# Kernel optimization log

Measured on AMD Instinct MI355X. Metric: run time of the kernel, lower is better.

The kernel has to match this reference:

```python
import jax, jax.numpy as jnp
import numpy as np

NEG_BIG = -9e15
ALPHA = 0.2  # LeakyReLU negative slope
B, N, F_IN, F_OUT = 8, 2048, 128, 128


def setup_inputs() -> dict:
    key = jax.random.key(0)
    k1, k2, k3, k4 = jax.random.split(key, 4)
    inp = jax.random.normal(k1, (B, N, F_IN), dtype=jnp.float32)
    adj = jax.random.randint(k2, (B, N, N), 0, 2, dtype=jnp.int32)
    W = 0.02 * jax.random.normal(k3, (F_OUT, F_IN), dtype=jnp.float32)  # nn.Linear weight [out,in]
    a = 0.02 * jax.random.normal(k4, (1, 2 * F_OUT), dtype=jnp.float32)  # attention vector [1, 2F]
    return {"input": inp, "adj": adj, "W": W, "a": a}


def reference(input, adj, W, a):
    # h = input @ W^T : [B, N, F_OUT]
    h = jnp.einsum("bnf,of->bno", input, W)
    f_out = h.shape[-1]
    # Decompose a . [h_i || h_j] = (h_i . a1) + (h_j . a2) -- same math as the
    # explicit repeat_interleave/repeat/cat, without the O(N^2 * 2F) tensor.
    a1 = a[0, :f_out]
    a2 = a[0, f_out:]
    s1 = h @ a1  # [B, N] score for source node i
    s2 = h @ a2  # [B, N] score for target node j
    e = jax.nn.leaky_relu(s1[:, :, None] + s2[:, None, :], negative_slope=ALPHA)  # [B,N,N]
    masked = jnp.where(adj > 0, e, NEG_BIG)
    attention = jax.nn.softmax(masked, axis=-1)
    # dropout p=0.0 (eval) -> identity
    h_prime = jnp.einsum("bnm,bmo->bno", attention, h)
    return h_prime
```

## Files before the change

### kernel.cpp

```cpp
#include <hip/hip_runtime.h>
#include <stdint.h>


#define B_ 8
#define N_ 2048
#define FD 128
#define ALPHA_ 0.2f
#define TJ 32
#define NCH 16
#define CHU4 512

typedef __attribute__((ext_vector_type(8))) short short8;
typedef __attribute__((ext_vector_type(4))) float f32x4;

#define HCHUNK(o, jc) ((((o) * 16) + ((jc) ^ ((o) & 15))) * 8)
#define U32(o, jc) (((o) >> 1) * 8 + ((((((o) & 1) << 2)) | (jc)) ^ (((o) >> 1) & 7)))

__device__ __forceinline__ float bf2f(unsigned short u) {
    union { uint32_t i; float f; } v; v.i = ((uint32_t)u) << 16; return v.f;
}
__device__ __forceinline__ unsigned short f2bf(float f) {
    union { float f; uint32_t i; } v; v.f = f;
    uint32_t x = v.i;
    uint32_t r = (x + 0x7fffu + ((x >> 16) & 1u)) >> 16;
    return (unsigned short)r;
}

__device__ __forceinline__ void gl2lds16(const uint4* g, uint4* l) {
    __builtin_amdgcn_global_load_lds(
        (const __attribute__((address_space(1))) uint32_t*)g,
        (__attribute__((address_space(3))) uint32_t*)l, 16, 0, 0);
}

__global__ __launch_bounds__(256) void gat_h(
    const float* __restrict__ x,
    const float* __restrict__ W,
    const float* __restrict__ a,
    unsigned short* __restrict__ hT,
    float* __restrict__ s1o, float* __restrict__ s2o)
{
    __shared__ __align__(16) unsigned short Wlds[FD * FD];

    const int bid = blockIdx.x;
    const int tid = threadIdx.x;
    const int w = tid >> 6;
    const int lane = tid & 63;
    const int m = lane & 15;
    const int quad = lane >> 4;
    const int arow = bid * 64 + w * 16 + m;

#pragma unroll
    for (int it = 0; it < 8; it++) {
        int cid = it * 256 + tid;
        int o = cid >> 4, kc = cid & 15;
        const float* wp = W + (size_t)o * FD + kc * 8;
        float4 w0 = *(const float4*)wp;
        float4 w1 = *(const float4*)(wp + 4);
        uint4 pk;
        pk.x = (uint32_t)f2bf(w0.x) | ((uint32_t)f2bf(w0.y) << 16);
        pk.y = (uint32_t)f2bf(w0.z) | ((uint32_t)f2bf(w0.w) << 16);
        pk.z = (uint32_t)f2bf(w1.x) | ((uint32_t)f2bf(w1.y) << 16);
        pk.w = (uint32_t)f2bf(w1.z) | ((uint32_t)f2bf(w1.w) << 16);
        *(uint4*)&Wlds[HCHUNK(o, kc)] = pk;
    }
    __syncthreads();

    f32x4 acc[8];
#pragma unroll
    for (int ot = 0; ot < 8; ot++) acc[ot] = (f32x4){0.f, 0.f, 0.f, 0.f};

#pragma unroll
    for (int ks = 0; ks < 4; ks++) {
        const float* xp = x + (size_t)arow * FD + ks * 32 + quad * 8;
        float4 x0 = *(const float4*)xp;
        float4 x1 = *(const float4*)(xp + 4);
        float xv[8] = {x0.x, x0.y, x0.z, x0.w, x1.x, x1.y, x1.z, x1.w};
        union { unsigned short us[8]; short8 v; } ahi, alo;
#pragma unroll
        for (int jj = 0; jj < 8; jj++) {
            unsigned short hi = f2bf(xv[jj]);
            ahi.us[jj] = hi;
            alo.us[jj] = f2bf(xv[jj] - bf2f(hi));
        }
#pragma unroll
        for (int ot = 0; ot < 8; ot++) {
            union { uint4 u; short8 v; } bw;
            bw.u = *(const uint4*)&Wlds[HCHUNK(ot * 16 + m, ks * 4 + quad)];
            acc[ot] = __builtin_amdgcn_mfma_f32_16x16x32_bf16(ahi.v, bw.v, acc[ot], 0, 0, 0);
            acc[ot] = __builtin_amdgcn_mfma_f32_16x16x32_bf16(alo.v, bw.v, acc[ot], 0, 0, 0);
        }
    }

    const int rc0 = bid * 64 + w * 16 + quad * 4;
    const int bb = rc0 >> 11;
    const int jb = rc0 & (N_ - 1);
    const int kc = jb >> 5;
    const int jc2 = (jb & 31) >> 3;
    const int off = jb & 7;
    unsigned short* hTb = hT + (size_t)bb * FD * N_ + (size_t)kc * (CHU4 * 8);
    float s1p[4] = {0.f, 0.f, 0.f, 0.f};
    float s2p[4] = {0.f, 0.f, 0.f, 0.f};
#pragma unroll
    for (int ot = 0; ot < 8; ot++) {
        const int o = ot * 16 + m;
        uint2 pk;
        pk.x = (uint32_t)f2bf(acc[ot][0]) | ((uint32_t)f2bf(acc[ot][1]) << 16);
        pk.y = (uint32_t)f2bf(acc[ot][2]) | ((uint32_t)f2bf(acc[ot][3]) << 16);
        *(uint2*)(hTb + (size_t)U32(o, jc2) * 8 + off) = pk;
        float a1v = a[o], a2v = a[FD + o];
#pragma unroll
        for (int r = 0; r < 4; r++) {
            s1p[r] += acc[ot][r] * a1v;
            s2p[r] += acc[ot][r] * a2v;
        }
    }
#pragma unroll
    for (int offx = 8; offx >= 1; offx >>= 1) {
#pragma unroll
        for (int r = 0; r < 4; r++) {
            s1p[r] += __shfl_xor(s1p[r], offx);
            s2p[r] += __shfl_xor(s2p[r], offx);
        }
    }
    if (m == 0) {
#pragma unroll
        for (int r = 0; r < 4; r++) {
            s1o[rc0 + r] = s1p[r];
            s2o[rc0 + r] = s2p[r];
        }
    }
}

__global__ __launch_bounds__(512, 4) void gat_attn(
    const int* __restrict__ adj,
    const unsigned short* __restrict__ hT,
    const float* __restrict__ s1,
    const float* __restrict__ s2,
    float* __restrict__ out)
{
    __shared__ __align__(16) uint4 hbuf[4][2][CHU4];
    __shared__ float rsq[4][2][16];

    const int bid = blockIdx.x;
    const int b = bid & 7;
    const int ib = bid >> 3;
    const int i0 = ib * 32;
    const int tid = threadIdx.x;
    const int lane = tid & 63;
    const int w = tid >> 6;
    const int rh = w & 1;
    const int jq = w >> 1;
    const int m = lane & 15;
    const int quad = lane >> 4;

    const int irow = i0 + rh * 16 + m;
    const float s1v = s1[b * N_ + irow];
    const int* adjrow = adj + ((size_t)(b * N_ + irow)) * N_ + jq * 512;
    const float* s2q = s2 + b * N_ + jq * 512;
    const uint4* hTq = (const uint4*)hT + (size_t)b * (FD * N_ / 8)
                       + (size_t)jq * NCH * CHU4;

#pragma unroll
    for (int q = 0; q < 4; q++)
        gl2lds16(&hTq[rh * 256 + q * 64 + lane], &hbuf[jq][0][rh * 256 + q * 64]);
    int4 a0 = *(const int4*)(adjrow + quad * 8);
    int4 a1 = *(const int4*)(adjrow + quad * 8 + 4);
    float4 sc0 = *(const float4*)(s2q + quad * 8);
    float4 sc1 = *(const float4*)(s2q + quad * 8 + 4);
    __syncthreads();

    f32x4 acc[8];
#pragma unroll
    for (int ot = 0; ot < 8; ot++) acc[ot] = (f32x4){0.f, 0.f, 0.f, 0.f};
    float rs_loc = 0.f;

    for (int k = 0; k < NCH; k++) {
        const int buf = k & 1;
        const bool more = (k + 1 < NCH);
        int4 na0, na1;
        float4 ns0, ns1;
        if (more) {
#pragma unroll
            for (int q = 0; q < 4; q++)
                gl2lds16(&hTq[(size_t)(k + 1) * CHU4 + rh * 256 + q * 64 + lane],
                         &hbuf[jq][buf ^ 1][rh * 256 + q * 64]);
            const int j1 = (k + 1) * TJ;
            na0 = *(const int4*)(adjrow + j1 + quad * 8);
            na1 = *(const int4*)(adjrow + j1 + quad * 8 + 4);
            ns0 = *(const float4*)(s2q + j1 + quad * 8);
            ns1 = *(const float4*)(s2q + j1 + quad * 8 + 4);
        }

        {
            float sarr[8] = {sc0.x, sc0.y, sc0.z, sc0.w, sc1.x, sc1.y, sc1.z, sc1.w};
            int aarr[8] = {a0.x, a0.y, a0.z, a0.w, a1.x, a1.y, a1.z, a1.w};
            union { unsigned short us[8]; short8 v; } af;
#pragma unroll
            for (int jj = 0; jj < 8; jj++) {
                float e = s1v + sarr[jj];
                e = (e > 0.f) ? e : (ALPHA_ * e);
                float p = (aarr[jj] > 0) ? __expf(e) : 0.f;
                rs_loc += p;
                af.us[jj] = f2bf(p);
            }
#pragma unroll
            for (int ot = 0; ot < 8; ot++) {
                const int o = ot * 16 + m;
                union { uint4 u; short8 v; } bf;
                bf.u = *(const uint4*)&hbuf[jq][buf][U32(o, quad)];
                acc[ot] = __builtin_amdgcn_mfma_f32_16x16x32_bf16(af.v, bf.v, acc[ot], 0, 0, 0);
            }
        }

        __syncthreads();
        if (more) { a0 = na0; a1 = na1; sc0 = ns0; sc1 = ns1; }
    }

    rs_loc += __shfl_xor(rs_loc, 16);
    rs_loc += __shfl_xor(rs_loc, 32);

    float* xch = (float*)&hbuf[0][0][0];
    if (jq != 0) {
#pragma unroll
        for (int ot = 0; ot < 8; ot++)
#pragma unroll
            for (int r = 0; r < 4; r++)
                xch[((jq - 1) * 32 + rh * 16 + quad * 4 + r) * 132 + ot * 16 + m]
                    = acc[ot][r];
        if (quad == 0) rsq[jq][rh][m] = rs_loc;
    }
    __syncthreads();
    if (jq == 0) {
        float rinv[4];
#pragma unroll
        for (int r = 0; r < 4; r++) {
            const int p = quad * 4 + r;
            float rtot = __shfl(rs_loc, p)
                       + rsq[1][rh][p] + rsq[2][rh][p] + rsq[3][rh][p];
            rinv[r] = 1.0f / rtot;
        }
        float* outp = out + (size_t)(b * N_ + i0 + rh * 16) * FD;
#pragma unroll
        for (int ot = 0; ot < 8; ot++) {
            const int col = ot * 16 + m;
#pragma unroll
            for (int r = 0; r < 4; r++) {
                const int row = rh * 16 + quad * 4 + r;
                float v = acc[ot][r]
                        + xch[(row) * 132 + col]
                        + xch[(32 + row) * 132 + col]
                        + xch[(64 + row) * 132 + col];
                outp[(size_t)(quad * 4 + r) * FD + col] = v * rinv[r];
            }
        }
    }
}

extern "C" void kernel_launch(void* const* d_in, const int* in_sizes, int n_in,
                              void* d_out, int out_size, void* d_ws, size_t ws_size,
                              hipStream_t stream) {
    const void* xv = d_in[0];
    const void* adjv = d_in[1];
    const void* Wv = d_in[2];
    const void* av = d_in[3];
    for (int i = 0; i < n_in; i++) {
        switch (in_sizes[i]) {
            case 2097152:  xv = d_in[i]; break;
            case 33554432: adjv = d_in[i]; break;
            case 16384:    Wv = d_in[i]; break;
            case 256:      av = d_in[i]; break;
            default: break;
        }
    }
    const float* x = (const float*)xv;
    const int* adj = (const int*)adjv;
    const float* W = (const float*)Wv;
    const float* a = (const float*)av;
    float* out = (float*)d_out;

    char* p = (char*)d_ws;
    unsigned short* hT = (unsigned short*)p;  p += (size_t)B_ * FD * N_ * 2;
    float* s1 = (float*)p;                    p += (size_t)B_ * N_ * 4;
    float* s2 = (float*)p;

    gat_h<<<256, 256, 0, stream>>>(x, W, a, hT, s1, s2);
    gat_attn<<<512, 512, 0, stream>>>(adj, hT, s1, s2, out);
}
```

Measured before the change: 216.2 us.

## Pre-pack adjacency into bitmasks and stage s2 scores in LDS

The h-projection kernel gains a pass that reads the full int32 adjacency matrix and packs it into 32-bit bitmasks in the workspace. The attention kernel then reads one word per 32 neighbours instead of 32 ints, and it loads the s2 scores for the batch into LDS once instead of prefetching them from global memory each chunk. This makes the attention loop much lighter on memory and registers. In exchange, the full adjacency read moves into a separate pass run by a small grid whose block count is limited by its shared-memory footprint, and it is no longer overlapped with the MFMA work.

```diff
diff --git a/kernel.cpp b/kernel.cpp
--- a/kernel.cpp
+++ b/kernel.cpp
@@ -36,8 +36,10 @@
     const float* __restrict__ x,
     const float* __restrict__ W,
     const float* __restrict__ a,
+    const int* __restrict__ adj,
     unsigned short* __restrict__ hT,
-    float* __restrict__ s1o, float* __restrict__ s2o)
+    float* __restrict__ s1o, float* __restrict__ s2o,
+    uint32_t* __restrict__ adjp)
 {
     __shared__ __align__(16) unsigned short Wlds[FD * FD];
 
@@ -129,16 +131,33 @@
             s2o[rc0 + r] = s2p[r];
         }
     }
+
+    const int tall = bid * 256 + tid;
+#pragma unroll 1
+    for (int it = 0; it < 16; it++) {
+        const int widx = it * 65536 + tall;
+        uint32_t bits = 0;
+#pragma unroll
+        for (int q = 0; q < 8; q++) {
+            int4 v = ((const int4*)adj)[(size_t)widx * 8 + q];
+            bits |= (v.x > 0 ? 1u : 0u) << (q * 4 + 0);
+            bits |= (v.y > 0 ? 1u : 0u) << (q * 4 + 1);
+            bits |= (v.z > 0 ? 1u : 0u) << (q * 4 + 2);
+            bits |= (v.w > 0 ? 1u : 0u) << (q * 4 + 3);
+        }
+        adjp[widx] = bits;
+    }
 }
 
 __global__ __launch_bounds__(512, 4) void gat_attn(
-    const int* __restrict__ adj,
+    const uint32_t* __restrict__ adjp,
     const unsigned short* __restrict__ hT,
     const float* __restrict__ s1,
     const float* __restrict__ s2,
     float* __restrict__ out)
 {
     __shared__ __align__(16) uint4 hbuf[4][2][CHU4];
+    __shared__ float s2lds[N_];
     __shared__ float rsq[4][2][16];
 
     const int bid = blockIdx.x;
@@ -155,18 +174,15 @@
 
     const int irow = i0 + rh * 16 + m;
     const float s1v = s1[b * N_ + irow];
-    const int* adjrow = adj + ((size_t)(b * N_ + irow)) * N_ + jq * 512;
-    const float* s2q = s2 + b * N_ + jq * 512;
+    const uint32_t* pwrow = adjp + ((size_t)(b * N_ + irow)) * (N_ / 32) + jq * NCH;
     const uint4* hTq = (const uint4*)hT + (size_t)b * (FD * N_ / 8)
                        + (size_t)jq * NCH * CHU4;
 
+    *(float4*)&s2lds[tid * 4] = *(const float4*)(s2 + b * N_ + tid * 4);
 #pragma unroll
     for (int q = 0; q < 4; q++)
         gl2lds16(&hTq[rh * 256 + q * 64 + lane], &hbuf[jq][0][rh * 256 + q * 64]);
-    int4 a0 = *(const int4*)(adjrow + quad * 8);
-    int4 a1 = *(const int4*)(adjrow + quad * 8 + 4);
-    float4 sc0 = *(const float4*)(s2q + quad * 8);
-    float4 sc1 = *(const float4*)(s2q + quad * 8 + 4);
+    uint32_t pw = pwrow[0];
     __syncthreads();
 
     f32x4 acc[8];
@@ -177,29 +193,27 @@
     for (int k = 0; k < NCH; k++) {
         const int buf = k & 1;
         const bool more = (k + 1 < NCH);
-        int4 na0, na1;
-        float4 ns0, ns1;
+        uint32_t npw = 0;
         if (more) {
 #pragma unroll
             for (int q = 0; q < 4; q++)
                 gl2lds16(&hTq[(size_t)(k + 1) * CHU4 + rh * 256 + q * 64 + lane],
                          &hbuf[jq][buf ^ 1][rh * 256 + q * 64]);
-            const int j1 = (k + 1) * TJ;
-            na0 = *(const int4*)(adjrow + j1 + quad * 8);
-            na1 = *(const int4*)(adjrow + j1 + quad * 8 + 4);
-            ns0 = *(const float4*)(s2q + j1 + quad * 8);
-            ns1 = *(const float4*)(s2q + j1 + quad * 8 + 4);
+            npw = pwrow[k + 1];
         }
 
         {
+            const float* sp = &s2lds[jq * 512 + k * TJ + quad * 8];
+            float4 sc0 = *(const float4*)sp;
+            float4 sc1 = *(const float4*)(sp + 4);
             float sarr[8] = {sc0.x, sc0.y, sc0.z, sc0.w, sc1.x, sc1.y, sc1.z, sc1.w};
-            int aarr[8] = {a0.x, a0.y, a0.z, a0.w, a1.x, a1.y, a1.z, a1.w};
+            const uint32_t bits = pw >> (quad * 8);
             union { unsigned short us[8]; short8 v; } af;
 #pragma unroll
             for (int jj = 0; jj < 8; jj++) {
                 float e = s1v + sarr[jj];
                 e = (e > 0.f) ? e : (ALPHA_ * e);
-                float p = (aarr[jj] > 0) ? __expf(e) : 0.f;
+                float p = ((bits >> jj) & 1u) ? __expf(e) : 0.f;
                 rs_loc += p;
                 af.us[jj] = f2bf(p);
             }
@@ -213,7 +227,7 @@
         }
 
         __syncthreads();
-        if (more) { a0 = na0; a1 = na1; sc0 = ns0; sc1 = ns1; }
+        if (more) pw = npw;
     }
 
     rs_loc += __shfl_xor(rs_loc, 16);
@@ -281,8 +295,9 @@
     char* p = (char*)d_ws;
     unsigned short* hT = (unsigned short*)p;  p += (size_t)B_ * FD * N_ * 2;
     float* s1 = (float*)p;                    p += (size_t)B_ * N_ * 4;
-    float* s2 = (float*)p;
-
-    gat_h<<<256, 256, 0, stream>>>(x, W, a, hT, s1, s2);
-    gat_attn<<<512, 512, 0, stream>>>(adj, hT, s1, s2, out);
-}
+    float* s2 = (float*)p;                    p += (size_t)B_ * N_ * 4;
+    uint32_t* adjp = (uint32_t*)p;
+
+    gat_h<<<256, 256, 0, stream>>>(x, W, a, adj, hT, s1, s2, adjp);
+    gat_attn<<<512, 512, 0, stream>>>(adjp, hT, s1, s2, out);
+}
```

New measurement: 259.0 us. 19.8% more time.
